# Kernel optimization log

Hardware: AMD Instinct MI355X
Metric: run time of the kernel (lower is better)

## Reference

```python
import jax, jax.numpy as jnp
import numpy as np

B, S, H, E, I, MAX_K, A_HID = 2, 2048, 1024, 8, 2688, 6, 50


def setup_inputs() -> dict:
    key = jax.random.key(0)
    ks = jax.random.split(key, 10)
    sc = 0.02
    return {
        "hidden_states": jax.random.normal(ks[0], (B, S, H), dtype=jnp.float32),
        "router_w": jax.random.normal(ks[1], (E, H), dtype=jnp.float32) * sc,
        "actor_w1": jax.random.normal(ks[2], (A_HID, H), dtype=jnp.float32) * sc,
        "actor_b1": jnp.zeros((A_HID,), dtype=jnp.float32),
        "actor_w2": jax.random.normal(ks[3], (MAX_K, A_HID), dtype=jnp.float32) * sc,
        "actor_b2": jnp.zeros((MAX_K,), dtype=jnp.float32),
        "gate_w": jax.random.normal(ks[4], (E, I, H), dtype=jnp.float32) * sc,
        "up_w": jax.random.normal(ks[5], (E, I, H), dtype=jnp.float32) * sc,
        "down_w": jax.random.normal(ks[6], (E, H, I), dtype=jnp.float32) * sc,
    }


def reference(hidden_states, router_w, actor_w1, actor_b1, actor_w2, actor_b2,
              gate_w, up_w, down_w):
    # Router: frozen linear -> softmax probs  [B,S,E]
    probs = jax.nn.softmax(
        jnp.einsum("bsh,eh->bse", hidden_states, router_w).astype(jnp.float32),
        axis=-1)

    # Allocator (ActorCritic.actor): Linear -> GELU -> Linear, clamp(-30,30)
    a_h = jax.nn.gelu(jnp.einsum("bsh,ah->bsa", hidden_states, actor_w1) + actor_b1)
    actor_logits = jnp.clip(
        jnp.einsum("bsa,ka->bsk", a_h, actor_w2) + actor_b2, -30.0, 30.0)
    # deterministic per-token k in [1, MAX_K]
    sampled_k = jnp.argmax(actor_logits, axis=-1) + 1  # [B,S] int

    # dynamic_topk_indices_and_scores: iterative argmax+scatter == select the
    # k highest-prob experts per token; keep their scores, zero elsewhere.
    order = jnp.argsort(-probs, axis=-1)           # descending order of experts
    rank = jnp.argsort(order, axis=-1)             # rank[e] = position of expert e
    mask = rank < sampled_k[..., None]             # [B,S,E] bool, top-k selected
    scores = jnp.where(mask, probs, 0.0).astype(hidden_states.dtype)

    # Expert dispatch-combine: out = sum_e scores[...,e] * LlamaMLP_e(x)
    out = jnp.zeros_like(hidden_states)
    for e in range(E):  # fixed small loop over experts
        g = jnp.einsum("bsh,ih->bsi", hidden_states, gate_w[e])
        u = jnp.einsum("bsh,ih->bsi", hidden_states, up_w[e])
        y = jnp.einsum("bsi,hi->bsh", jax.nn.silu(g) * u, down_w[e])
        out = out + scores[..., e:e + 1] * y
    return out
```

## Files before the change

kernel.cpp:

```cpp
#include <hip/hip_runtime.h>
#include <hip/hip_bf16.h>
#include <stdint.h>

#define TOK 4096
#define HD  1024
#define NE  8
#define ID  2688
#define MAXK 6
#define AHID 50
#define NROW 58
#define KCH 64
#define NCH (HD / KCH)

#define BM 128
#define BN 128
#define BK 64
#define NTM (TOK / BM)
#define NTN_GU (ID / BN)
#define NB_GU (NTN_GU * NTM)
#define NTN_D (HD / BN)
#define NB_D (NTN_D * NTM)

typedef float  f32x4  __attribute__((ext_vector_type(4)));
typedef __bf16 bf16x8 __attribute__((ext_vector_type(8)));
typedef ushort ushort8v __attribute__((ext_vector_type(8)));

__device__ __forceinline__ ushort f2bf(float f) {
  union { float f; uint32_t u; } v; v.f = f;
  return (ushort)((v.u + 0x7FFFu + ((v.u >> 16) & 1u)) >> 16);
}
__device__ __forceinline__ float bf2f(ushort u) {
  union { uint32_t u; float f; } v; v.u = (uint32_t)u << 16; return v.f;
}

#define GLD_LDS16(gp, lp)                                                      \
  __builtin_amdgcn_global_load_lds(                                            \
      (const __attribute__((address_space(1))) uint32_t*)(uintptr_t)(gp),      \
      (__attribute__((address_space(3))) uint32_t*)(uint32_t)(uintptr_t)(lp),  \
      16, 0, 0)

__global__ void k_cvt(const float* __restrict__ src, ushort* __restrict__ dst, int n) {
  int idx = blockIdx.x * blockDim.x + threadIdx.x;
  int stride = gridDim.x * blockDim.x;
  for (int i = idx * 8; i < n; i += stride * 8) {
    float4 a = *(const float4*)(src + i);
    float4 b = *(const float4*)(src + i + 4);
    ushort8v o;
    o[0] = f2bf(a.x); o[1] = f2bf(a.y); o[2] = f2bf(a.z); o[3] = f2bf(a.w);
    o[4] = f2bf(b.x); o[5] = f2bf(b.y); o[6] = f2bf(b.z); o[7] = f2bf(b.w);
    *(ushort8v*)(dst + i) = o;
  }
}

__global__ __launch_bounds__(256) void k_logits(
    const float* __restrict__ x, const float* __restrict__ rw,
    const float* __restrict__ aw1, float* __restrict__ partial,
    ushort* __restrict__ Xb) {
  __shared__ float xs[256][KCH + 1];
  const int tid = threadIdx.x;
  const int t0 = blockIdx.x * 256;
  const int c = blockIdx.y;
  const int k0 = c * KCH;
#pragma unroll
  for (int j = 0; j < 16; ++j) {
    const int id4 = j * 256 + tid;
    const int row = id4 >> 4;
    const int c4 = (id4 & 15) * 4;
    float4 v = *(const float4*)(x + (size_t)(t0 + row) * HD + k0 + c4);
    xs[row][c4 + 0] = v.x; xs[row][c4 + 1] = v.y;
    xs[row][c4 + 2] = v.z; xs[row][c4 + 3] = v.w;
    ushort4 o; o.x = f2bf(v.x); o.y = f2bf(v.y); o.z = f2bf(v.z); o.w = f2bf(v.w);
    *(ushort4*)(Xb + (size_t)(t0 + row) * HD + k0 + c4) = o;
  }
  __syncthreads();
  float acc[NROW];
#pragma unroll
  for (int r = 0; r < NROW; ++r) acc[r] = 0.f;
  for (int k4 = 0; k4 < KCH; k4 += 4) {
    const float x0 = xs[tid][k4 + 0], x1 = xs[tid][k4 + 1];
    const float x2 = xs[tid][k4 + 2], x3 = xs[tid][k4 + 3];
#pragma unroll
    for (int r = 0; r < NROW; ++r) {
      const float* wp = ((r < NE) ? (rw + (size_t)r * HD)
                                  : (aw1 + (size_t)(r - NE) * HD)) + k0 + k4;
      acc[r] += x0 * wp[0] + x1 * wp[1] + x2 * wp[2] + x3 * wp[3];
    }
  }
  const int t = t0 + tid;
#pragma unroll
  for (int r = 0; r < NROW; ++r)
    partial[((size_t)c * NROW + r) * TOK + t] = acc[r];
}

__global__ __launch_bounds__(256) void k_reduce(
    const float* __restrict__ partial, float* __restrict__ dots) {
  const int t = blockIdx.x * 256 + threadIdx.x;
  const int r = blockIdx.y;
  float s = 0.f;
#pragma unroll
  for (int c = 0; c < NCH; ++c)
    s += partial[((size_t)c * NROW + r) * TOK + t];
  dots[(size_t)r * TOK + t] = s;
}

__global__ __launch_bounds__(64) void k_select(
    const float* __restrict__ dots, const float* __restrict__ ab1_,
    const float* __restrict__ aw2_, const float* __restrict__ ab2_,
    float* __restrict__ scores, int* __restrict__ idx, int* __restrict__ cnt) {
  const int lane = threadIdx.x;
  const int t = blockIdx.x * 64 + lane;
  float d[NROW];
#pragma unroll
  for (int r = 0; r < NROW; ++r) d[r] = dots[(size_t)r * TOK + t];
  float m = d[0];
#pragma unroll
  for (int e = 1; e < NE; ++e) m = fmaxf(m, d[e]);
  float p[NE]; float sum = 0.f;
#pragma unroll
  for (int e = 0; e < NE; ++e) { p[e] = expf(d[e] - m); sum += p[e]; }
  float inv = 1.f / sum;
#pragma unroll
  for (int e = 0; e < NE; ++e) p[e] *= inv;
  float lg[MAXK];
#pragma unroll
  for (int k = 0; k < MAXK; ++k) lg[k] = ab2_[k];
#pragma unroll
  for (int i = 0; i < AHID; ++i) {
    float v = d[NE + i] + ab1_[i];
    float g = 0.5f * v * (1.f + tanhf(0.7978845608028654f * (v + 0.044715f * v * v * v)));
#pragma unroll
    for (int k = 0; k < MAXK; ++k) lg[k] += g * aw2_[k * AHID + i];
  }
  int best = 0; float bv = fminf(fmaxf(lg[0], -30.f), 30.f);
#pragma unroll
  for (int k = 1; k < MAXK; ++k) {
    float lv = fminf(fmaxf(lg[k], -30.f), 30.f);
    if (lv > bv) { bv = lv; best = k; }
  }
  const int kk = best + 1;
  float sc[NE];
#pragma unroll
  for (int e = 0; e < NE; ++e) {
    int rank = 0;
#pragma unroll
    for (int j = 0; j < NE; ++j)
      rank += (p[j] > p[e]) || (p[j] == p[e] && j < e);
    sc[e] = (rank < kk) ? p[e] : 0.f;
    scores[(size_t)t * NE + e] = sc[e];
  }
#pragma unroll
  for (int e = 0; e < NE; ++e) {
    unsigned long long msk = __ballot(sc[e] > 0.f);
    int npop = __popcll(msk);
    int mypos = __popcll(msk & ((1ull << lane) - 1ull));
    int base = 0;
    if (lane == 0 && npop) base = atomicAdd(cnt + e, npop);
    base = __shfl(base, 0);
    if (sc[e] > 0.f) idx[e * TOK + base + mypos] = t;
  }
}

__global__ __launch_bounds__(256, 2) void k_gateup(
    const ushort* __restrict__ X, const int* __restrict__ idx,
    const int* __restrict__ cnt,
    const ushort* __restrict__ Wg, const ushort* __restrict__ Wu,
    ushort* __restrict__ act, const int e0, const int actStrideRows) {
  __shared__ __attribute__((aligned(16))) ushort As[BM * BK];
  __shared__ __attribute__((aligned(16))) ushort Bg[BN * BK];
  __shared__ __attribute__((aligned(16))) ushort Bu[BN * BK];

  const int e = e0 + blockIdx.z;
  const int n = cnt[e];
  const int bid = blockIdx.x;
  const int logical = (bid & 7) * (NB_GU / 8) + (bid >> 3);
  const int tn = logical >> 5;
  const int tm = logical & (NTM - 1);
  const int row0 = tm * BM;
  if (row0 >= n) return;
  const int* idx_e = idx + e * TOK;
  const ushort* WgE = Wg + (size_t)e * ID * HD;
  const ushort* WuE = Wu + (size_t)e * ID * HD;
  ushort* actE = act + (size_t)actStrideRows * e * ID;

  const int tid = threadIdx.x;
  const int lane = tid & 63;
  const int w = tid >> 6;
  const int wr = (w >> 1) * 64;
  const int wc = (w & 1) * 64;
  const int srow = lane >> 3;
  const int scol = (lane & 7) * 8;
  const int col0 = tn * BN;

  f32x4 accg[4][4] = {};
  f32x4 accu[4][4] = {};

  const ushort* pa[4]; const ushort* pg[4]; const ushort* pu[4];
  ushort* la[4]; ushort* lg[4]; ushort* lu[4];
#pragma unroll
  for (int j = 0; j < 4; ++j) {
    const int cc = w * 4 + j;
    const int r = cc * 8 + srow;
    const int token = idx_e[min(row0 + r, n - 1)];
    pa[j] = X   + (size_t)token * HD + scol;
    pg[j] = WgE + (size_t)(col0 + r) * HD + scol;
    pu[j] = WuE + (size_t)(col0 + r) * HD + scol;
    la[j] = &As[cc * 512]; lg[j] = &Bg[cc * 512]; lu[j] = &Bu[cc * 512];
  }

  for (int kt = 0; kt < HD / BK; ++kt) {
    const int k0 = kt * BK;
    __syncthreads();
#pragma unroll
    for (int j = 0; j < 4; ++j) {
      GLD_LDS16(pa[j] + k0, la[j]);
      GLD_LDS16(pg[j] + k0, lg[j]);
      GLD_LDS16(pu[j] + k0, lu[j]);
    }
    __syncthreads();
#pragma unroll
    for (int kk = 0; kk < 2; ++kk) {
      const int kc = kk * 32 + (lane >> 4) * 8;
      const int rr = lane & 15;
      bf16x8 af[4], gf[4], uf[4];
#pragma unroll
      for (int m = 0; m < 4; ++m)
        af[m] = *(const bf16x8*)&As[(wr + m * 16 + rr) * BK + kc];
#pragma unroll
      for (int nn = 0; nn < 4; ++nn) {
        gf[nn] = *(const bf16x8*)&Bg[(wc + nn * 16 + rr) * BK + kc];
        uf[nn] = *(const bf16x8*)&Bu[(wc + nn * 16 + rr) * BK + kc];
      }
#pragma unroll
      for (int m = 0; m < 4; ++m)
#pragma unroll
        for (int nn = 0; nn < 4; ++nn) {
          accg[m][nn] = __builtin_amdgcn_mfma_f32_16x16x32_bf16(af[m], gf[nn], accg[m][nn], 0, 0, 0);
          accu[m][nn] = __builtin_amdgcn_mfma_f32_16x16x32_bf16(af[m], uf[nn], accu[m][nn], 0, 0, 0);
        }
    }
  }
  const int erow = (lane >> 4) * 4;
  const int ecol = lane & 15;
#pragma unroll
  for (int m = 0; m < 4; ++m) {
    const int gr = row0 + wr + m * 16 + erow;
#pragma unroll
    for (int nn = 0; nn < 4; ++nn) {
      const int gc = col0 + wc + nn * 16 + ecol;
#pragma unroll
      for (int j = 0; j < 4; ++j) {
        float g = accg[m][nn][j];
        float u = accu[m][nn][j];
        float h = (g / (1.f + __expf(-g))) * u;
        actE[(size_t)(gr + j) * ID + gc] = f2bf(h);
      }
    }
  }
}

__global__ __launch_bounds__(256, 2) void k_down(
    const ushort* __restrict__ act, const ushort* __restrict__ Wd,
    const int* __restrict__ idx, const int* __restrict__ cnt,
    ushort* __restrict__ y) {
  __shared__ __attribute__((aligned(16))) ushort As[BM * BK];
  __shared__ __attribute__((aligned(16))) ushort Bs[BN * BK];

  const int e = blockIdx.z;
  const int n = cnt[e];
  const int bid = blockIdx.x;
  const int logical = (bid & 7) * (NB_D / 8) + (bid >> 3);
  const int tn = logical >> 5;
  const int tm = logical & (NTM - 1);
  const int row0 = tm * BM;
  if (row0 >= n) return;
  const int* idx_e = idx + e * TOK;
  const ushort* A = act + (size_t)e * TOK * ID;
  const ushort* W = Wd + (size_t)e * HD * ID;
  ushort* yE = y + (size_t)e * TOK * HD;

  const int tid = threadIdx.x;
  const int lane = tid & 63;
  const int w = tid >> 6;
  const int wr = (w >> 1) * 64;
  const int wc = (w & 1) * 64;
  const int srow = lane >> 3;
  const int scol = (lane & 7) * 8;
  const int col0 = tn * BN;

  f32x4 acc[4][4] = {};

  const ushort* pa[4]; const ushort* pb[4];
  ushort* la[4]; ushort* lb[4];
#pragma unroll
  for (int j = 0; j < 4; ++j) {
    const int cc = w * 4 + j;
    const int r = cc * 8 + srow;
    pa[j] = A + (size_t)min(row0 + r, n - 1) * ID + scol;
    pb[j] = W + (size_t)(col0 + r) * ID + scol;
    la[j] = &As[cc * 512]; lb[j] = &Bs[cc * 512];
  }

  for (int kt = 0; kt < ID / BK; ++kt) {
    const int k0 = kt * BK;
    __syncthreads();
#pragma unroll
    for (int j = 0; j < 4; ++j) {
      GLD_LDS16(pa[j] + k0, la[j]);
      GLD_LDS16(pb[j] + k0, lb[j]);
    }
    __syncthreads();
#pragma unroll
    for (int kk = 0; kk < 2; ++kk) {
      const int kc = kk * 32 + (lane >> 4) * 8;
      const int rr = lane & 15;
      bf16x8 af[4], bf_[4];
#pragma unroll
      for (int m = 0; m < 4; ++m)
        af[m] = *(const bf16x8*)&As[(wr + m * 16 + rr) * BK + kc];
#pragma unroll
      for (int nn = 0; nn < 4; ++nn)
        bf_[nn] = *(const bf16x8*)&Bs[(wc + nn * 16 + rr) * BK + kc];
#pragma unroll
      for (int m = 0; m < 4; ++m)
#pragma unroll
        for (int nn = 0; nn < 4; ++nn)
          acc[m][nn] = __builtin_amdgcn_mfma_f32_16x16x32_bf16(af[m], bf_[nn], acc[m][nn], 0, 0, 0);
    }
  }

  const int erow = (lane >> 4) * 4, ecol = lane & 15;
#pragma unroll
  for (int m = 0; m < 4; ++m) {
    const int cr0 = row0 + wr + m * 16 + erow;
#pragma unroll
    for (int j = 0; j < 4; ++j) {
      const int cr = cr0 + j;
      if (cr < n) {
        const int token = idx_e[cr];
        ushort* yp = yE + (size_t)token * HD + col0 + wc;
#pragma unroll
        for (int nn = 0; nn < 4; ++nn)
          yp[nn * 16 + ecol] = f2bf(acc[m][nn][j]);
      }
    }
  }
}

__global__ __launch_bounds__(256) void k_combine(
    const ushort* __restrict__ y, const float* __restrict__ scores,
    float* __restrict__ out) {
  const int w = threadIdx.x >> 6, lane = threadIdx.x & 63;
  const int t = blockIdx.x * 4 + w;
  const int c0 = lane * 16;
  float acc[16];
#pragma unroll
  for (int i = 0; i < 16; ++i) acc[i] = 0.f;
  const float* sc = scores + (size_t)t * NE;
#pragma unroll
  for (int e = 0; e < NE; ++e) {
    const float s = sc[e];
    if (s > 0.f) {
      const ushort8v* yp = (const ushort8v*)(y + ((size_t)e * TOK + t) * HD + c0);
      ushort8v v0 = yp[0], v1 = yp[1];
#pragma unroll
      for (int i = 0; i < 8; ++i) acc[i] += s * bf2f(v0[i]);
#pragma unroll
      for (int i = 0; i < 8; ++i) acc[8 + i] += s * bf2f(v1[i]);
    }
  }
  float* op = out + (size_t)t * HD + c0;
#pragma unroll
  for (int i = 0; i < 4; ++i)
    *(float4*)(op + 4 * i) = make_float4(acc[4*i], acc[4*i+1], acc[4*i+2], acc[4*i+3]);
}

__global__ __launch_bounds__(256) void k_down64(
    const ushort* __restrict__ act, const ushort* __restrict__ Wd,
    const float* __restrict__ scores, const int* __restrict__ idx,
    const int* __restrict__ cnt, const int e, float* __restrict__ out) {
  __shared__ __attribute__((aligned(16))) ushort As[64 * 64];
  __shared__ __attribute__((aligned(16))) ushort Bs[64 * 64];
  const int n = cnt[e];
  const int row0 = blockIdx.y * 64;
  if (row0 >= n) return;
  const int* idx_e = idx + e * TOK;
  const ushort* A = act;
  const ushort* W = Wd + (size_t)e * HD * ID;
  const int col0 = blockIdx.x * 64;
  const int tid = threadIdx.x, lane = tid & 63, w = tid >> 6;
  const int wr = (w >> 1) * 32, wc = (w & 1) * 32;
  const int srow = lane >> 3, scol = (lane & 7) * 8;
  f32x4 acc[2][2] = {};
  const ushort* pa[2]; const ushort* pb[2];
  ushort* la[2]; ushort* lb[2];
#pragma unroll
  for (int j = 0; j < 2; ++j) {
    const int cc = w * 2 + j;
    const int r = cc * 8 + srow;
    pa[j] = A + (size_t)min(row0 + r, n - 1) * ID + scol;
    pb[j] = W + (size_t)(col0 + r) * ID + scol;
    la[j] = &As[cc * 512]; lb[j] = &Bs[cc * 512];
  }
  for (int kt = 0; kt < ID / 64; ++kt) {
    const int k0 = kt * 64;
    __syncthreads();
#pragma unroll
    for (int j = 0; j < 2; ++j) { GLD_LDS16(pa[j] + k0, la[j]); GLD_LDS16(pb[j] + k0, lb[j]); }
    __syncthreads();
#pragma unroll
    for (int kk = 0; kk < 2; ++kk) {
      const int kc = kk * 32 + (lane >> 4) * 8;
      const int rr = lane & 15;
      bf16x8 af[2], bf_[2];
#pragma unroll
      for (int m = 0; m < 2; ++m) af[m] = *(const bf16x8*)&As[(wr + m * 16 + rr) * 64 + kc];
#pragma unroll
      for (int nn = 0; nn < 2; ++nn) bf_[nn] = *(const bf16x8*)&Bs[(wc + nn * 16 + rr) * 64 + kc];
#pragma unroll
      for (int m = 0; m < 2; ++m)
#pragma unroll
        for (int nn = 0; nn < 2; ++nn)
          acc[m][nn] = __builtin_amdgcn_mfma_f32_16x16x32_bf16(af[m], bf_[nn], acc[m][nn], 0, 0, 0);
    }
  }
  const int erow = (lane >> 4) * 4, ecol = lane & 15;
#pragma unroll
  for (int m = 0; m < 2; ++m) {
    const int cr0 = row0 + wr + m * 16 + erow;
#pragma unroll
    for (int j = 0; j < 4; ++j) {
      const int cr = cr0 + j;
      if (cr < n) {
        const int token = idx_e[cr];
        const float s = scores[(size_t)token * NE + e];
        float* op = out + (size_t)token * HD + col0 + wc;
#pragma unroll
        for (int nn = 0; nn < 2; ++nn) op[nn * 16 + ecol] += s * acc[m][nn][j];
      }
    }
  }
}

extern "C" void kernel_launch(void* const* d_in, const int* in_sizes, int n_in,
                              void* d_out, int out_size, void* d_ws, size_t ws_size,
                              hipStream_t stream) {
  const float* hs       = (const float*)d_in[0];
  const float* router_w = (const float*)d_in[1];
  const float* actor_w1 = (const float*)d_in[2];
  const float* actor_b1 = (const float*)d_in[3];
  const float* actor_w2 = (const float*)d_in[4];
  const float* actor_b2 = (const float*)d_in[5];
  const float* gate_w   = (const float*)d_in[6];
  const float* up_w     = (const float*)d_in[7];
  const float* down_w   = (const float*)d_in[8];
  float* out = (float*)d_out;

  const size_t sz_x    = (size_t)TOK * HD * 2;
  const size_t sz_w    = (size_t)NE * ID * HD * 2;
  const size_t sz_act1 = (size_t)TOK * ID * 2;
  const size_t sz_actC = (size_t)NE * TOK * ID * 2;
  const size_t sz_part = (size_t)NCH * NROW * TOK * 4;
  const size_t sz_dt   = (size_t)NROW * TOK * 4;
  const size_t sz_sc   = (size_t)TOK * NE * 4;
  const size_t sz_ix   = (size_t)NE * TOK * 4;

  const size_t fixed = sz_x + 3 * sz_w;
  const size_t tail  = sz_dt + sz_sc + sz_ix + 256;
  const size_t fb_act = (sz_act1 > sz_part ? sz_act1 : sz_part);
  const size_t need_fb = fixed + fb_act + tail;
  const size_t need_cb = fixed + sz_actC + tail;
  if (ws_size < need_fb) return;
  const bool combined = (ws_size >= need_cb);
  const size_t act_sz = combined ? sz_actC : fb_act;

  char* ws = (char*)d_ws;
  ushort* Xb  = (ushort*)ws;
  ushort* Wgb = (ushort*)(ws + sz_x);
  ushort* Wub = (ushort*)(ws + sz_x + sz_w);
  ushort* Wdb = (ushort*)(ws + sz_x + 2 * sz_w);
  ushort* yb  = Wgb;
  ushort* act = (ushort*)(ws + fixed);
  float*  partial = (float*)(ws + fixed);
  float*  dots   = (float*)(ws + fixed + act_sz);
  float*  scores = (float*)(ws + fixed + act_sz + sz_dt);
  int*    idx    = (int*)  (ws + fixed + act_sz + sz_dt + sz_sc);
  int*    cnt    = (int*)  (ws + fixed + act_sz + sz_dt + sz_sc + sz_ix);

  hipMemsetAsync(cnt, 0, NE * 4, stream);

  k_cvt<<<2048, 256, 0, stream>>>(gate_w, Wgb, NE * ID * HD);
  k_cvt<<<2048, 256, 0, stream>>>(up_w,   Wub, NE * ID * HD);
  k_cvt<<<2048, 256, 0, stream>>>(down_w, Wdb, NE * ID * HD);

  k_logits<<<dim3(TOK / 256, NCH), 256, 0, stream>>>(hs, router_w, actor_w1, partial, Xb);
  k_reduce<<<dim3(TOK / 256, NROW), 256, 0, stream>>>(partial, dots);
  k_select<<<TOK / 64, 64, 0, stream>>>(dots, actor_b1, actor_w2, actor_b2,
                                        scores, idx, cnt);

  if (combined) {
    k_gateup<<<dim3(NB_GU, 1, NE), 256, 0, stream>>>(
        Xb, idx, cnt, Wgb, Wub, act, 0, TOK);
    k_down<<<dim3(NB_D, 1, NE), 256, 0, stream>>>(act, Wdb, idx, cnt, yb);
    k_combine<<<TOK / 4, 256, 0, stream>>>(yb, scores, out);
  } else {
    hipMemsetAsync(out, 0, (size_t)TOK * HD * 4, stream);
    for (int e = 0; e < NE; ++e) {
      k_gateup<<<dim3(NB_GU, 1, 1), 256, 0, stream>>>(
          Xb, idx, cnt, Wgb, Wub, act, e, 0);
      k_down64<<<dim3(HD / 64, TOK / 64), 256, 0, stream>>>(
          act, Wdb, scores, idx, cnt, e, out);
    }
  }
}
```

Measured before the change: 551.8 us.

## Interleave gate/up weights and compute gate-up as one fused GEMM with LDS exchange

Converts gate and up weights into a single interleaved bf16 matrix in which every 128-row block holds 64 gate rows followed by 64 up rows. The gate-up kernel then runs a single 128x128 GEMM per tile with half the accumulators and B-tile LDS. Odd warps pass their up-projection results to even warps through LDS for the SiLU*up epilogue. The goal is lower register and LDS pressure and possibly higher occupancy, at the cost of twice as many blocks, re-reading the A tile per block, and an extra LDS exchange with barriers.

Result: faster. 520.8 us (-5.6%).

```diff
diff --git a/kernel.cpp b/kernel.cpp
--- a/kernel.cpp
+++ b/kernel.cpp
@@ -16,8 +16,9 @@
 #define BN 128
 #define BK 64
 #define NTM (TOK / BM)
-#define NTN_GU (ID / BN)
-#define NB_GU (NTN_GU * NTM)
+#define NID2 (2 * ID)
+#define NTN_GUC (NID2 / BN)
+#define NB_GUC (NTN_GUC * NTM)
 #define NTN_D (HD / BN)
 #define NB_D (NTN_D * NTM)
 
@@ -52,6 +53,28 @@
   }
 }
 
+__global__ void k_cvt_gu(const float* __restrict__ g, const float* __restrict__ u,
+                         ushort* __restrict__ dst) {
+  const int total = NE * NID2 * (HD / 8);
+  int idx = blockIdx.x * blockDim.x + threadIdx.x;
+  int stride = gridDim.x * blockDim.x;
+  for (int i8 = idx; i8 < total; i8 += stride) {
+    const int col = (i8 & (HD / 8 - 1)) * 8;
+    const int row = i8 >> 7;
+    const int e = row / NID2;
+    const int q = row - e * NID2;
+    const int p = q >> 7, r = q & 127;
+    const float* src = ((r < 64) ? g + ((size_t)e * ID + p * 64 + r) * HD
+                                 : u + ((size_t)e * ID + p * 64 + (r - 64)) * HD) + col;
+    float4 a = *(const float4*)(src);
+    float4 b = *(const float4*)(src + 4);
+    ushort8v o;
+    o[0] = f2bf(a.x); o[1] = f2bf(a.y); o[2] = f2bf(a.z); o[3] = f2bf(a.w);
+    o[4] = f2bf(b.x); o[5] = f2bf(b.y); o[6] = f2bf(b.z); o[7] = f2bf(b.w);
+    *(ushort8v*)(dst + (size_t)row * HD + col) = o;
+  }
+}
+
 __global__ __launch_bounds__(256) void k_logits(
     const float* __restrict__ x, const float* __restrict__ rw,
     const float* __restrict__ aw1, float* __restrict__ partial,
@@ -160,26 +183,24 @@
   }
 }
 
-__global__ __launch_bounds__(256, 2) void k_gateup(
+__global__ __launch_bounds__(256, 2) void k_gateupC(
     const ushort* __restrict__ X, const int* __restrict__ idx,
-    const int* __restrict__ cnt,
-    const ushort* __restrict__ Wg, const ushort* __restrict__ Wu,
+    const int* __restrict__ cnt, const ushort* __restrict__ Wc,
     ushort* __restrict__ act, const int e0, const int actStrideRows) {
-  __shared__ __attribute__((aligned(16))) ushort As[BM * BK];
-  __shared__ __attribute__((aligned(16))) ushort Bg[BN * BK];
-  __shared__ __attribute__((aligned(16))) ushort Bu[BN * BK];
+  __shared__ __attribute__((aligned(16))) ushort lds[BM * BK + BN * BK];
+  ushort* As = lds;
+  ushort* Bs = lds + BM * BK;
 
   const int e = e0 + blockIdx.z;
   const int n = cnt[e];
   const int bid = blockIdx.x;
-  const int logical = (bid & 7) * (NB_GU / 8) + (bid >> 3);
+  const int logical = (bid & 7) * (NB_GUC / 8) + (bid >> 3);
   const int tn = logical >> 5;
   const int tm = logical & (NTM - 1);
   const int row0 = tm * BM;
   if (row0 >= n) return;
   const int* idx_e = idx + e * TOK;
-  const ushort* WgE = Wg + (size_t)e * ID * HD;
-  const ushort* WuE = Wu + (size_t)e * ID * HD;
+  const ushort* WcE = Wc + (size_t)e * NID2 * HD;
   ushort* actE = act + (size_t)actStrideRows * e * ID;
 
   const int tid = threadIdx.x;
@@ -191,20 +212,18 @@
   const int scol = (lane & 7) * 8;
   const int col0 = tn * BN;
 
-  f32x4 accg[4][4] = {};
-  f32x4 accu[4][4] = {};
-
-  const ushort* pa[4]; const ushort* pg[4]; const ushort* pu[4];
-  ushort* la[4]; ushort* lg[4]; ushort* lu[4];
+  f32x4 acc[4][4] = {};
+
+  const ushort* pa[4]; const ushort* pb[4];
+  ushort* la[4]; ushort* lb[4];
 #pragma unroll
   for (int j = 0; j < 4; ++j) {
     const int cc = w * 4 + j;
     const int r = cc * 8 + srow;
     const int token = idx_e[min(row0 + r, n - 1)];
     pa[j] = X   + (size_t)token * HD + scol;
-    pg[j] = WgE + (size_t)(col0 + r) * HD + scol;
-    pu[j] = WuE + (size_t)(col0 + r) * HD + scol;
-    la[j] = &As[cc * 512]; lg[j] = &Bg[cc * 512]; lu[j] = &Bu[cc * 512];
+    pb[j] = WcE + (size_t)(col0 + r) * HD + scol;
+    la[j] = &As[cc * 512]; lb[j] = &Bs[cc * 512];
   }
 
   for (int kt = 0; kt < HD / BK; ++kt) {
@@ -213,46 +232,60 @@
 #pragma unroll
     for (int j = 0; j < 4; ++j) {
       GLD_LDS16(pa[j] + k0, la[j]);
-      GLD_LDS16(pg[j] + k0, lg[j]);
-      GLD_LDS16(pu[j] + k0, lu[j]);
+      GLD_LDS16(pb[j] + k0, lb[j]);
     }
     __syncthreads();
 #pragma unroll
     for (int kk = 0; kk < 2; ++kk) {
       const int kc = kk * 32 + (lane >> 4) * 8;
       const int rr = lane & 15;
-      bf16x8 af[4], gf[4], uf[4];
+      bf16x8 af[4], bf_[4];
 #pragma unroll
       for (int m = 0; m < 4; ++m)
         af[m] = *(const bf16x8*)&As[(wr + m * 16 + rr) * BK + kc];
 #pragma unroll
+      for (int nn = 0; nn < 4; ++nn)
+        bf_[nn] = *(const bf16x8*)&Bs[(wc + nn * 16 + rr) * BK + kc];
+#pragma unroll
+      for (int m = 0; m < 4; ++m)
+#pragma unroll
+        for (int nn = 0; nn < 4; ++nn)
+          acc[m][nn] = __builtin_amdgcn_mfma_f32_16x16x32_bf16(af[m], bf_[nn], acc[m][nn], 0, 0, 0);
+    }
+  }
+
+  const int erow = (lane >> 4) * 4, ecol = lane & 15;
+  float* exch = (float*)lds;
+  __syncthreads();
+  if (w & 1) {
+#pragma unroll
+    for (int m = 0; m < 4; ++m) {
+      const int rbase = wr + m * 16 + erow;
+#pragma unroll
       for (int nn = 0; nn < 4; ++nn) {
-        gf[nn] = *(const bf16x8*)&Bg[(wc + nn * 16 + rr) * BK + kc];
-        uf[nn] = *(const bf16x8*)&Bu[(wc + nn * 16 + rr) * BK + kc];
+        const int c = nn * 16 + ecol;
+#pragma unroll
+        for (int j = 0; j < 4; ++j)
+          exch[(rbase + j) * 64 + c] = acc[m][nn][j];
       }
-#pragma unroll
-      for (int m = 0; m < 4; ++m)
-#pragma unroll
-        for (int nn = 0; nn < 4; ++nn) {
-          accg[m][nn] = __builtin_amdgcn_mfma_f32_16x16x32_bf16(af[m], gf[nn], accg[m][nn], 0, 0, 0);
-          accu[m][nn] = __builtin_amdgcn_mfma_f32_16x16x32_bf16(af[m], uf[nn], accu[m][nn], 0, 0, 0);
+    }
+  }
+  __syncthreads();
+  if (!(w & 1)) {
+#pragma unroll
+    for (int m = 0; m < 4; ++m) {
+      const int rbase = wr + m * 16 + erow;
+#pragma unroll
+      for (int nn = 0; nn < 4; ++nn) {
+        const int c = nn * 16 + ecol;
+        const int gc = tn * 64 + c;
+#pragma unroll
+        for (int j = 0; j < 4; ++j) {
+          float g = acc[m][nn][j];
+          float u = exch[(rbase + j) * 64 + c];
+          float h = (g / (1.f + __expf(-g))) * u;
+          actE[(size_t)(row0 + rbase + j) * ID + gc] = f2bf(h);
         }
-    }
-  }
-  const int erow = (lane >> 4) * 4;
-  const int ecol = lane & 15;
-#pragma unroll
-  for (int m = 0; m < 4; ++m) {
-    const int gr = row0 + wr + m * 16 + erow;
-#pragma unroll
-    for (int nn = 0; nn < 4; ++nn) {
-      const int gc = col0 + wc + nn * 16 + ecol;
-#pragma unroll
-      for (int j = 0; j < 4; ++j) {
-        float g = accg[m][nn][j];
-        float u = accu[m][nn][j];
-        float h = (g / (1.f + __expf(-g))) * u;
-        actE[(size_t)(gr + j) * ID + gc] = f2bf(h);
       }
     }
   }
@@ -457,6 +490,7 @@
 
   const size_t sz_x    = (size_t)TOK * HD * 2;
   const size_t sz_w    = (size_t)NE * ID * HD * 2;
+  const size_t sz_wgu  = 2 * sz_w;
   const size_t sz_act1 = (size_t)TOK * ID * 2;
   const size_t sz_actC = (size_t)NE * TOK * ID * 2;
   const size_t sz_part = (size_t)NCH * NROW * TOK * 4;
@@ -464,7 +498,7 @@
   const size_t sz_sc   = (size_t)TOK * NE * 4;
   const size_t sz_ix   = (size_t)NE * TOK * 4;
 
-  const size_t fixed = sz_x + 3 * sz_w;
+  const size_t fixed = sz_x + sz_wgu + sz_w;
   const size_t tail  = sz_dt + sz_sc + sz_ix + 256;
   const size_t fb_act = (sz_act1 > sz_part ? sz_act1 : sz_part);
   const size_t need_fb = fixed + fb_act + tail;
@@ -475,10 +509,9 @@
 
   char* ws = (char*)d_ws;
   ushort* Xb  = (ushort*)ws;
-  ushort* Wgb = (ushort*)(ws + sz_x);
-  ushort* Wub = (ushort*)(ws + sz_x + sz_w);
-  ushort* Wdb = (ushort*)(ws + sz_x + 2 * sz_w);
-  ushort* yb  = Wgb;
+  ushort* Wgu = (ushort*)(ws + sz_x);
+  ushort* Wdb = (ushort*)(ws + sz_x + sz_wgu);
+  ushort* yb  = Wgu;
   ushort* act = (ushort*)(ws + fixed);
   float*  partial = (float*)(ws + fixed);
   float*  dots   = (float*)(ws + fixed + act_sz);
@@ -488,8 +521,7 @@
 
   hipMemsetAsync(cnt, 0, NE * 4, stream);
 
-  k_cvt<<<2048, 256, 0, stream>>>(gate_w, Wgb, NE * ID * HD);
-  k_cvt<<<2048, 256, 0, stream>>>(up_w,   Wub, NE * ID * HD);
+  k_cvt_gu<<<2048, 256, 0, stream>>>(gate_w, up_w, Wgu);
   k_cvt<<<2048, 256, 0, stream>>>(down_w, Wdb, NE * ID * HD);
 
   k_logits<<<dim3(TOK / 256, NCH), 256, 0, stream>>>(hs, router_w, actor_w1, partial, Xb);
@@ -498,15 +530,15 @@
                                         scores, idx, cnt);
 
   if (combined) {
-    k_gateup<<<dim3(NB_GU, 1, NE), 256, 0, stream>>>(
-        Xb, idx, cnt, Wgb, Wub, act, 0, TOK);
+    k_gateupC<<<dim3(NB_GUC, 1, NE), 256, 0, stream>>>(
+        Xb, idx, cnt, Wgu, act, 0, TOK);
     k_down<<<dim3(NB_D, 1, NE), 256, 0, stream>>>(act, Wdb, idx, cnt, yb);
     k_combine<<<TOK / 4, 256, 0, stream>>>(yb, scores, out);
   } else {
     hipMemsetAsync(out, 0, (size_t)TOK * HD * 4, stream);
     for (int e = 0; e < NE; ++e) {
-      k_gateup<<<dim3(NB_GU, 1, 1), 256, 0, stream>>>(
-          Xb, idx, cnt, Wgb, Wub, act, e, 0);
+      k_gateupC<<<dim3(NB_GUC, 1, 1), 256, 0, stream>>>(
+          Xb, idx, cnt, Wgu, act, e, 0);
       k_down64<<<dim3(HD / 64, TOK / 64), 256, 0, stream>>>(
           act, Wdb, scores, idx, cnt, e, out);
     }
```
